# Optimization experiments

Measured on AMD Instinct MI355X. Metric: run time of the kernel, lower is better.

## Reference

```python
import jax, jax.numpy as jnp
import numpy as np

# The original module calls an opaque CPU extension (pixel_cluster_cpu.forward)
# performing offset-guided pixel grouping. This reference implements the
# standard vectorized semantics of such post-processing:
#  - valid pixels = non_zeros_map > 0 and pixel_gt > 0 (foreground instances)
#  - instance-balanced per-pixel weights: w = 1 / |instance| for valid pixels
#  - each pixel follows its predicted offset (dy, dx) to a target pixel; the
#    offset is 'correct' if the target belongs to the same gt instance
#  - pixel_weight  = w * sigmoid(pixel_pred)                  (B, R, C)
#  - offset_weight = (correct * w) * offset_pred              (B, 2, R, C)

MAX_INSTANCES = 16  # pixel_gt ids in [0, MAX_INSTANCES), 0 = background


def _cluster(non_zeros_map, pixel_pred, offset_pred, pixel_gt):
    B, R, C = pixel_gt.shape
    dt = pixel_pred.dtype
    mask = (non_zeros_map > 0) & (pixel_gt > 0)              # (B,R,C) bool
    maskf = mask.astype(dt)

    # instance sizes per batch element -> instance-balanced weights
    flat_gt = pixel_gt.reshape(B, -1)                        # (B, R*C)
    sizes = jax.vmap(
        lambda g, m: jax.ops.segment_sum(m, g, num_segments=MAX_INSTANCES)
    )(flat_gt, maskf.reshape(B, -1))                         # (B, MAX_INSTANCES)
    inv_size = 1.0 / jnp.maximum(sizes, 1.0)
    w = jnp.take_along_axis(inv_size, flat_gt, axis=1).reshape(B, R, C) * maskf

    # follow offsets: target pixel = round((r,c) + (dy,dx)), clipped to image
    rr = jnp.arange(R, dtype=dt)[:, None]                    # (R,1)
    cc = jnp.arange(C, dtype=dt)[None, :]                    # (1,C)
    ty = jnp.clip(jnp.round(rr + offset_pred[:, 0]), 0, R - 1).astype(jnp.int32)
    tx = jnp.clip(jnp.round(cc + offset_pred[:, 1]), 0, C - 1).astype(jnp.int32)
    gt_at_target = jax.vmap(lambda g, y, x: g[y, x])(pixel_gt, ty, tx)  # (B,R,C)
    agree = ((gt_at_target == pixel_gt) & mask).astype(dt)

    pixel_weight = w * jax.nn.sigmoid(pixel_pred)            # (B,R,C)
    offset_weight = (agree * w)[:, None] * offset_pred       # (B,2,R,C)
    return pixel_weight, offset_weight


def setup_inputs() -> dict:
    key = jax.random.key(0)
    k1, k2, k3, k4 = jax.random.split(key, 4)
    B, R, C = 8, 1024, 1024
    non_zeros_map = jax.random.randint(k1, (B, R, C), 0, 2).astype(jnp.int32)
    pixel_pred = jax.random.normal(k2, (B, R, C), dtype=jnp.float32)
    offset_pred = jax.random.normal(k3, (B, 2, R, C), dtype=jnp.float32) * 4.0
    pixel_gt = jax.random.randint(k4, (B, R, C), 0, MAX_INSTANCES).astype(jnp.int32)
    return {
        "non_zeros_map": non_zeros_map,
        "pixel_pred": pixel_pred,
        "offset_pred": offset_pred,
        "pixel_gt": pixel_gt,
    }


def reference(non_zeros_map, pixel_pred, offset_pred, pixel_gt):
    return _cluster(non_zeros_map, pixel_pred, offset_pred, pixel_gt)
```

## Files before the change

kernel.cpp:

```cpp
#include <hip/hip_runtime.h>
#include <cstdint>
#include <cstddef>

#define NB   8
#define RDIM 1024
#define CDIM 1024
#define PB   (RDIM * CDIM)
#define NI   16

typedef int     i32x4 __attribute__((ext_vector_type(4)));
typedef float   f32x4 __attribute__((ext_vector_type(4)));
typedef uint8_t u8x4  __attribute__((ext_vector_type(4)));

__global__ __launch_bounds__(256) void count_pack_kernel(
    const int* __restrict__ nz, const int* __restrict__ gt,
    uint8_t* __restrict__ gt8, int* __restrict__ counts)
{
    __shared__ unsigned s[4 * NI];
    const int b    = blockIdx.y;
    const int lane = threadIdx.x & 63;
    const int wv   = threadIdx.x >> 6;
    const i32x4* nzb = (const i32x4*)(nz + (size_t)b * PB);
    const i32x4* gtb = (const i32x4*)(gt + (size_t)b * PB);
    u8x4* g8b = gt8 ? (u8x4*)(gt8 + (size_t)b * PB) : nullptr;

    unsigned wc[NI];
    #pragma unroll
    for (int k = 0; k < NI; ++k) wc[k] = 0;

    const int n4 = PB / 4;
    for (int i = blockIdx.x * blockDim.x + threadIdx.x; i < n4;
         i += gridDim.x * blockDim.x) {
        i32x4 nzv = __builtin_nontemporal_load(&nzb[i]);
        i32x4 gv  = __builtin_nontemporal_load(&gtb[i]);
        int gm[4];
        u8x4 o;
        #pragma unroll
        for (int j = 0; j < 4; ++j) {
            const int g = gv[j];
            const int m = (nzv[j] > 0) & (g > 0);
            gm[j] = m ? g : 0;
            o[j]  = (uint8_t)(g | (m << 7));
        }
        if (g8b) g8b[i] = o;
        #pragma unroll
        for (int j = 0; j < 4; ++j) {
            #pragma unroll
            for (int id = 1; id < NI; ++id) {
                unsigned long long bal = __ballot(gm[j] == id);
                wc[id] += (unsigned)__popcll(bal);
            }
        }
    }
    if (lane == 0) {
        #pragma unroll
        for (int id = 1; id < NI; ++id) s[wv * NI + id] = wc[id];
    }
    __syncthreads();
    if (threadIdx.x >= 1 && threadIdx.x < NI) {
        unsigned sum = s[threadIdx.x] + s[NI + threadIdx.x] +
                       s[2 * NI + threadIdx.x] + s[3 * NI + threadIdx.x];
        if (sum) atomicAdd((unsigned*)&counts[b * NI + threadIdx.x], sum);
    }
}

template <bool PACKED>
__global__ __launch_bounds__(256) void cluster_kernel(
    const float* __restrict__ pp, const float* __restrict__ op,
    const uint8_t* __restrict__ gt8,
    const int* __restrict__ nz, const int* __restrict__ gt,
    const int* __restrict__ counts, float* __restrict__ out)
{
    __shared__ float inv[NI];
    const int b = blockIdx.y;
    if (threadIdx.x < NI) {
        int c = counts[b * NI + threadIdx.x];
        inv[threadIdx.x] = 1.0f / (float)(c > 1 ? c : 1);
    }
    __syncthreads();

    const int nbx = gridDim.x;
    const int p   = blockIdx.x;
    const int bx  = (p & 7) * (nbx >> 3) + (p >> 3);
    const int i   = bx * blockDim.x + threadIdx.x;

    const uint8_t* g8b = PACKED ? gt8 + (size_t)b * PB : nullptr;
    const int*     gtb = gt + (size_t)b * PB;
    const int*     nzb = nz + (size_t)b * PB;
    const float*   ppb = pp + (size_t)b * PB;
    const float*   dyb = op + (size_t)b * 2 * PB;
    const float*   dxb = dyb + PB;
    float* pwb  = out + (size_t)b * PB;
    float* owyb = out + (size_t)NB * PB + (size_t)b * 2 * PB;
    float* owxb = owyb + PB;

    const int   pix = i * 4;
    const float rf  = (float)(pix >> 10);
    const float cf0 = (float)(pix & (CDIM - 1));

    f32x4 ppv = __builtin_nontemporal_load((const f32x4*)ppb + i);
    f32x4 dyv = __builtin_nontemporal_load((const f32x4*)dyb + i);
    f32x4 dxv = __builtin_nontemporal_load((const f32x4*)dxb + i);

    int gs[4], ms[4];
    if (PACKED) {
        u8x4 gv = *((const u8x4*)g8b + i);
        #pragma unroll
        for (int j = 0; j < 4; ++j) { gs[j] = gv[j] & 0x7f; ms[j] = gv[j] >> 7; }
    } else {
        i32x4 gv  = *((const i32x4*)gtb + i);
        i32x4 nzv = *((const i32x4*)nzb + i);
        #pragma unroll
        for (int j = 0; j < 4; ++j) { gs[j] = gv[j]; ms[j] = (nzv[j] > 0) & (gv[j] > 0); }
    }

    f32x4 pwv, oyv, oxv;
    #pragma unroll
    for (int j = 0; j < 4; ++j) {
        const float dy = dyv[j], dx = dxv[j];
        const float w  = ms[j] ? inv[gs[j]] : 0.0f;
        float ty = fminf(fmaxf(rintf(rf + dy), 0.0f), (float)(RDIM - 1));
        float tx = fminf(fmaxf(rintf(cf0 + (float)j + dx), 0.0f), (float)(CDIM - 1));
        const int ti = (int)ty * CDIM + (int)tx;
        int tg;
        if (PACKED) tg = g8b[ti] & 0x7f;
        else        tg = gtb[ti];
        const float aw = (ms[j] && (tg == gs[j])) ? w : 0.0f;
        pwv[j] = w * (1.0f / (1.0f + __expf(-ppv[j])));
        oyv[j] = aw * dy;
        oxv[j] = aw * dx;
    }

    __builtin_nontemporal_store(pwv, (f32x4*)pwb  + i);
    __builtin_nontemporal_store(oyv, (f32x4*)owyb + i);
    __builtin_nontemporal_store(oxv, (f32x4*)owxb + i);
}

extern "C" void kernel_launch(void* const* d_in, const int* in_sizes, int n_in,
                              void* d_out, int out_size, void* d_ws, size_t ws_size,
                              hipStream_t stream) {
    const int*   nz = (const int*)d_in[0];
    const float* pp = (const float*)d_in[1];
    const float* op = (const float*)d_in[2];
    const int*   gt = (const int*)d_in[3];
    float* out = (float*)d_out;

    int* counts = (int*)d_ws;
    const size_t need = 1024 + (size_t)NB * PB;
    const bool packed = ws_size >= need;
    uint8_t* gt8 = packed ? (uint8_t*)d_ws + 1024 : nullptr;

    hipMemsetAsync(counts, 0, NB * NI * sizeof(int), stream);

    dim3 blkA(256), grdA(256, NB);
    count_pack_kernel<<<grdA, blkA, 0, stream>>>(nz, gt, gt8, counts);

    dim3 blkB(256), grdB(1024, NB);
    if (packed)
        cluster_kernel<true><<<grdB, blkB, 0, stream>>>(pp, op, gt8, nz, gt, counts, out);
    else
        cluster_kernel<false><<<grdB, blkB, 0, stream>>>(pp, op, nullptr, nz, gt, counts, out);
}
```

Baseline: 230.7 us.

## Stage packed gt row window into LDS for offset-target lookups

The cluster kernel now uses 1024-thread blocks that each handle 8 rows. Each block copies the packed gt bytes for those rows plus a 26-row margin into shared memory, and offset-target lookups read from LDS, falling back to global memory only when the target lies outside the window. This is meant to replace scattered global byte gathers with LDS reads. The cost is a large LDS footprint (about 60 KB per block), a staging copy that re-reads overlapping rows, and a barrier before compute, all of which could limit occupancy.

```diff
diff --git a/kernel.cpp b/kernel.cpp
--- a/kernel.cpp
+++ b/kernel.cpp
@@ -7,6 +7,10 @@
 #define CDIM 1024
 #define PB   (RDIM * CDIM)
 #define NI   16
+
+#define MARG  26
+#define BROWS 8
+#define WROWS (BROWS + 2 * MARG)
 
 typedef int     i32x4 __attribute__((ext_vector_type(4)));
 typedef float   f32x4 __attribute__((ext_vector_type(4)));
@@ -64,10 +68,98 @@
     }
 }
 
-template <bool PACKED>
-__global__ __launch_bounds__(256) void cluster_kernel(
+__global__ __launch_bounds__(1024, 8) void cluster_lds_kernel(
     const float* __restrict__ pp, const float* __restrict__ op,
     const uint8_t* __restrict__ gt8,
+    const int* __restrict__ counts, float* __restrict__ out)
+{
+    __shared__ __align__(16) uint8_t sg[WROWS * CDIM];
+    __shared__ float inv[NI];
+
+    const int b   = blockIdx.y;
+    const int tid = threadIdx.x;
+
+    const int nbx = gridDim.x;
+    const int p0  = blockIdx.x;
+    const int bx  = (p0 & 7) * (nbx >> 3) + (p0 >> 3);
+
+    const int r0 = bx * BROWS;
+    const int w0 = (r0 - MARG) > 0 ? (r0 - MARG) : 0;
+    int w1 = r0 + BROWS + MARG; if (w1 > RDIM) w1 = RDIM;
+
+    const uint8_t* g8b = gt8 + (size_t)b * PB;
+
+    if (tid < NI) {
+        int c = counts[b * NI + tid];
+        inv[tid] = 1.0f / (float)(c > 1 ? c : 1);
+    }
+    {
+        const int nb16 = ((w1 - w0) << 10) >> 4;
+        const i32x4* src = (const i32x4*)(g8b + ((size_t)w0 << 10));
+        i32x4* dst = (i32x4*)sg;
+        for (int k = tid; k < nb16; k += 1024) dst[k] = src[k];
+    }
+    __syncthreads();
+
+    const f32x4* ppb = (const f32x4*)(pp + (size_t)b * PB);
+    const f32x4* dyb = (const f32x4*)(op + (size_t)b * 2 * PB);
+    const f32x4* dxb = dyb + PB / 4;
+    f32x4* pwb  = (f32x4*)(out + (size_t)b * PB);
+    f32x4* owyb = (f32x4*)(out + (size_t)NB * PB + (size_t)b * 2 * PB);
+    f32x4* owxb = owyb + PB / 4;
+
+    const int q0 = bx * (BROWS * CDIM / 4) + tid;
+
+    f32x4 dyv[2], dxv[2], ppv[2];
+    #pragma unroll
+    for (int u = 0; u < 2; ++u) dyv[u] = __builtin_nontemporal_load(dyb + q0 + 1024 * u);
+    #pragma unroll
+    for (int u = 0; u < 2; ++u) dxv[u] = __builtin_nontemporal_load(dxb + q0 + 1024 * u);
+    #pragma unroll
+    for (int u = 0; u < 2; ++u) ppv[u] = __builtin_nontemporal_load(ppb + q0 + 1024 * u);
+
+    uint32_t own[2];
+    #pragma unroll
+    for (int u = 0; u < 2; ++u) {
+        const int pix = (q0 + 1024 * u) * 4;
+        const int r = pix >> 10, c = pix & (CDIM - 1);
+        own[u] = *(const uint32_t*)&sg[((r - w0) << 10) + c];
+    }
+
+    #pragma unroll
+    for (int u = 0; u < 2; ++u) {
+        const int   pix = (q0 + 1024 * u) * 4;
+        const float rf  = (float)(pix >> 10);
+        const float cf0 = (float)(pix & (CDIM - 1));
+        f32x4 pwv, oyv, oxv;
+        #pragma unroll
+        for (int j = 0; j < 4; ++j) {
+            const int gbyte = (own[u] >> (8 * j)) & 0xff;
+            const int gs = gbyte & 0x7f;
+            const int ms = gbyte >> 7;
+            const float dy = dyv[u][j], dx = dxv[u][j];
+            const float tyf = fminf(fmaxf(rintf(rf + dy), 0.0f), (float)(RDIM - 1));
+            const float txf = fminf(fmaxf(rintf(cf0 + (float)j + dx), 0.0f), (float)(CDIM - 1));
+            const int ty = (int)tyf, tx = (int)txf;
+            int tg;
+            if (ty >= w0 && ty < w1)
+                tg = sg[((ty - w0) << 10) + tx] & 0x7f;
+            else
+                tg = g8b[(ty << 10) + tx] & 0x7f;
+            const float w  = ms ? inv[gs] : 0.0f;
+            const float aw = (ms && (tg == gs)) ? w : 0.0f;
+            pwv[j] = w * (1.0f / (1.0f + __expf(-ppv[u][j])));
+            oyv[j] = aw * dy;
+            oxv[j] = aw * dx;
+        }
+        __builtin_nontemporal_store(pwv, pwb  + q0 + 1024 * u);
+        __builtin_nontemporal_store(oyv, owyb + q0 + 1024 * u);
+        __builtin_nontemporal_store(oxv, owxb + q0 + 1024 * u);
+    }
+}
+
+__global__ __launch_bounds__(256) void cluster_plain_kernel(
+    const float* __restrict__ pp, const float* __restrict__ op,
     const int* __restrict__ nz, const int* __restrict__ gt,
     const int* __restrict__ counts, float* __restrict__ out)
 {
@@ -78,62 +170,38 @@
         inv[threadIdx.x] = 1.0f / (float)(c > 1 ? c : 1);
     }
     __syncthreads();
-
-    const int nbx = gridDim.x;
-    const int p   = blockIdx.x;
-    const int bx  = (p & 7) * (nbx >> 3) + (p >> 3);
-    const int i   = bx * blockDim.x + threadIdx.x;
-
-    const uint8_t* g8b = PACKED ? gt8 + (size_t)b * PB : nullptr;
-    const int*     gtb = gt + (size_t)b * PB;
-    const int*     nzb = nz + (size_t)b * PB;
-    const float*   ppb = pp + (size_t)b * PB;
-    const float*   dyb = op + (size_t)b * 2 * PB;
-    const float*   dxb = dyb + PB;
-    float* pwb  = out + (size_t)b * PB;
-    float* owyb = out + (size_t)NB * PB + (size_t)b * 2 * PB;
-    float* owxb = owyb + PB;
+    const int i = blockIdx.x * blockDim.x + threadIdx.x;
+
+    const int*   gtb = gt + (size_t)b * PB;
+    const int*   nzb = nz + (size_t)b * PB;
+    const f32x4* ppb = (const f32x4*)(pp + (size_t)b * PB);
+    const f32x4* dyb = (const f32x4*)(op + (size_t)b * 2 * PB);
+    const f32x4* dxb = dyb + PB / 4;
+    f32x4* pwb  = (f32x4*)(out + (size_t)b * PB);
+    f32x4* owyb = (f32x4*)(out + (size_t)NB * PB + (size_t)b * 2 * PB);
+    f32x4* owxb = owyb + PB / 4;
 
     const int   pix = i * 4;
     const float rf  = (float)(pix >> 10);
     const float cf0 = (float)(pix & (CDIM - 1));
-
-    f32x4 ppv = __builtin_nontemporal_load((const f32x4*)ppb + i);
-    f32x4 dyv = __builtin_nontemporal_load((const f32x4*)dyb + i);
-    f32x4 dxv = __builtin_nontemporal_load((const f32x4*)dxb + i);
-
-    int gs[4], ms[4];
-    if (PACKED) {
-        u8x4 gv = *((const u8x4*)g8b + i);
-        #pragma unroll
-        for (int j = 0; j < 4; ++j) { gs[j] = gv[j] & 0x7f; ms[j] = gv[j] >> 7; }
-    } else {
-        i32x4 gv  = *((const i32x4*)gtb + i);
-        i32x4 nzv = *((const i32x4*)nzb + i);
-        #pragma unroll
-        for (int j = 0; j < 4; ++j) { gs[j] = gv[j]; ms[j] = (nzv[j] > 0) & (gv[j] > 0); }
-    }
+    f32x4 ppv = ppb[i], dyv = dyb[i], dxv = dxb[i];
+    i32x4 gv = *((const i32x4*)gtb + i), nzv = *((const i32x4*)nzb + i);
 
     f32x4 pwv, oyv, oxv;
     #pragma unroll
     for (int j = 0; j < 4; ++j) {
-        const float dy = dyv[j], dx = dxv[j];
-        const float w  = ms[j] ? inv[gs[j]] : 0.0f;
-        float ty = fminf(fmaxf(rintf(rf + dy), 0.0f), (float)(RDIM - 1));
-        float tx = fminf(fmaxf(rintf(cf0 + (float)j + dx), 0.0f), (float)(CDIM - 1));
-        const int ti = (int)ty * CDIM + (int)tx;
-        int tg;
-        if (PACKED) tg = g8b[ti] & 0x7f;
-        else        tg = gtb[ti];
-        const float aw = (ms[j] && (tg == gs[j])) ? w : 0.0f;
+        const int gs = gv[j];
+        const int ms = (nzv[j] > 0) & (gs > 0);
+        float ty = fminf(fmaxf(rintf(rf + dyv[j]), 0.0f), (float)(RDIM - 1));
+        float tx = fminf(fmaxf(rintf(cf0 + (float)j + dxv[j]), 0.0f), (float)(CDIM - 1));
+        const int tg = gtb[(int)ty * CDIM + (int)tx];
+        const float w  = ms ? inv[gs] : 0.0f;
+        const float aw = (ms && (tg == gs)) ? w : 0.0f;
         pwv[j] = w * (1.0f / (1.0f + __expf(-ppv[j])));
-        oyv[j] = aw * dy;
-        oxv[j] = aw * dx;
-    }
-
-    __builtin_nontemporal_store(pwv, (f32x4*)pwb  + i);
-    __builtin_nontemporal_store(oyv, (f32x4*)owyb + i);
-    __builtin_nontemporal_store(oxv, (f32x4*)owxb + i);
+        oyv[j] = aw * dyv[j];
+        oxv[j] = aw * dxv[j];
+    }
+    pwb[i] = pwv; owyb[i] = oyv; owxb[i] = oxv;
 }
 
 extern "C" void kernel_launch(void* const* d_in, const int* in_sizes, int n_in,
@@ -155,9 +223,12 @@
     dim3 blkA(256), grdA(256, NB);
     count_pack_kernel<<<grdA, blkA, 0, stream>>>(nz, gt, gt8, counts);
 
-    dim3 blkB(256), grdB(1024, NB);
-    if (packed)
-        cluster_kernel<true><<<grdB, blkB, 0, stream>>>(pp, op, gt8, nz, gt, counts, out);
-    else
-        cluster_kernel<false><<<grdB, blkB, 0, stream>>>(pp, op, nullptr, nz, gt, counts, out);
-}
+    if (packed) {
+        dim3 blkB(1024), grdB(RDIM / BROWS / 1, NB);
+        cluster_lds_kernel<<<dim3(128, NB), blkB, 0, stream>>>(pp, op, gt8, counts, out);
+        (void)grdB;
+    } else {
+        dim3 blkB(256), grdB(1024, NB);
+        cluster_plain_kernel<<<grdB, blkB, 0, stream>>>(pp, op, nz, gt, counts, out);
+    }
+}
```

Measured after the change: 227.5 us. About the same (-1.4%).
